# Optimization experiments

Hardware: AMD Instinct MI355X
Metric: run time of the kernel (lower is better)

Reference implementation:

```python
import jax, jax.numpy as jnp
import numpy as np

B = 4096          # batch_size * world_size
D = 256           # embedding dim
TEMP = 0.5        # temperature
EPS = 1e-8        # torch CosineSimilarity eps


def setup_inputs() -> dict:
    key = jax.random.key(0)
    k1, k2 = jax.random.split(key)
    z_i = jax.random.normal(k1, (B, D), dtype=jnp.float32)
    z_j = jax.random.normal(k2, (B, D), dtype=jnp.float32)
    return {"z_i": z_i, "z_j": z_j}


def reference(z_i, z_j):
    N = 2 * B
    z = jnp.concatenate([z_i, z_j], axis=0)                      # [N, D]
    # Cosine similarity: normalize rows (clamped norm like torch eps), then matmul.
    norms = jnp.maximum(jnp.linalg.norm(z, axis=1, keepdims=True), EPS)
    zn = z / norms
    sim = jnp.matmul(zn, zn.T) / TEMP                            # [N, N]
    # Positive pairs: offsets +B and -B from the diagonal.
    pos = jnp.concatenate([jnp.diagonal(sim, B), jnp.diagonal(sim, -B)])  # [N]
    # Cross-entropy with label 0 over [pos, negatives]:
    # logsumexp over {pos} U {negatives} == logsumexp over row excluding the diagonal
    # (the (i, i±B) entries removed by the mask are exactly re-added as the positive).
    neg_inf = jnp.array(-jnp.inf, dtype=sim.dtype)
    sim_nodiag = jnp.where(jnp.eye(N, dtype=bool), neg_inf, sim)
    lse = jax.nn.logsumexp(sim_nodiag, axis=1)                   # [N]
    loss = jnp.sum(lse - pos) / N                                # reduction='sum' then /N
    return loss
```

## Files before the change

### kernel.cpp

```cpp
#include <hip/hip_runtime.h>

#define NROWS 8192
#define DIM   256
#define BHALF 4096
#define NCHUNK 8
#define SCALE 1.69864358f
#define LN2F  0.69314718f

typedef unsigned char u8;
typedef __attribute__((ext_vector_type(4))) float f32x4;
typedef __attribute__((ext_vector_type(4))) int   i32x4;
typedef __attribute__((ext_vector_type(8))) int   i32x8;

__device__ inline void gload_lds16(const void* g, void* l) {
  __builtin_amdgcn_global_load_lds(
      (const __attribute__((address_space(1))) void*)g,
      (__attribute__((address_space(3))) void*)l, 16, 0, 0);
}

__global__ __launch_bounds__(256) void nrm_kernel(const float* __restrict__ zi,
                                                  const float* __restrict__ zj,
                                                  u8* __restrict__ zn8,
                                                  float* __restrict__ out) {
  if (blockIdx.x == 0 && threadIdx.x == 0) out[0] = 0.f;
  const int w = threadIdx.x >> 6, l = threadIdx.x & 63;
  const int row = blockIdx.x * 4 + w;
  const float* src = (row < BHALF) ? zi + (size_t)row * DIM
                                   : zj + (size_t)(row - BHALF) * DIM;
  float4 v = *(const float4*)(src + l * 4);
  float ss = v.x * v.x + v.y * v.y + v.z * v.z + v.w * v.w;
#pragma unroll
  for (int m = 1; m < 64; m <<= 1) ss += __shfl_xor(ss, m);
  float inv = SCALE / fmaxf(sqrtf(ss), 1e-8f);
  int p = __builtin_amdgcn_cvt_pk_fp8_f32(v.x * inv, v.y * inv, 0, false);
  p = __builtin_amdgcn_cvt_pk_fp8_f32(v.z * inv, v.w * inv, p, true);
  *(int*)(zn8 + (size_t)row * DIM + (size_t)l * 4) = p;
}

__global__ __launch_bounds__(256, 2) void sim_kernel(const u8* __restrict__ zn8,
                                                     float* __restrict__ partials,
                                                     float* __restrict__ pos) {
  __shared__ __align__(16) u8 Bsm[2][128 * DIM];
  __shared__ float plane[2][128];

  const int t = threadIdx.x;
  const int w = t >> 6, l = t & 63;
  const int wa = w >> 1, wb = w & 1;
  const int rl = l & 15, kg = l >> 4;

  const int rp = (int)blockIdx.x >> 3;
  const int ch = (int)blockIdx.x & 7;
  const int colbase = ch * 1024;

  int soff[8], doff[8];
#pragma unroll
  for (int i = 0; i < 8; ++i) {
    int c = i * 256 + t;
    int r = c >> 4, cd = c & 15;
    int cs = (cd & 8) | ((cd ^ r) & 7);
    soff[i] = r * DIM + cs * 16;
    doff[i] = (i * 256 + w * 64) * 16;
  }
  auto STAGE = [&](int base_row, u8* dst) {
#pragma unroll
    for (int i = 0; i < 8; ++i)
      gload_lds16(zn8 + (size_t)base_row * DIM + soff[i], dst + doff[i]);
  };
  auto RD2 = [&](const u8* buf, int row, i32x8* dst) {
    const int salt = row & 7;
    const u8* base = buf + row * DIM;
#pragma unroll
    for (int k = 0; k < 2; ++k) {
      i32x4 lo = *(const i32x4*)(base + ((k * 8 + ((kg * 2) ^ salt)) << 4));
      i32x4 hi = *(const i32x4*)(base + ((k * 8 + ((kg * 2 + 1) ^ salt)) << 4));
      dst[k] = __builtin_shufflevector(lo, hi, 0, 1, 2, 3, 4, 5, 6, 7);
    }
  };

  STAGE(rp * 128, &Bsm[0][0]);
  STAGE(colbase, &Bsm[1][0]);
  asm volatile("s_waitcnt vmcnt(8)" ::: "memory");
  __builtin_amdgcn_sched_barrier(0);
  __builtin_amdgcn_s_barrier();
  __builtin_amdgcn_sched_barrier(0);

  i32x8 pb[4][2];
#pragma unroll
  for (int pj = 0; pj < 4; ++pj)
    RD2(&Bsm[0][0], wb * 64 + pj * 16 + rl, pb[pj]);
  asm volatile("s_waitcnt lgkmcnt(0)" ::: "memory");
  __builtin_amdgcn_sched_barrier(0);

  const int dtile = ((rp >> 3) == ch) ? (rp & 7) : -1;
  const int pg = (rp < 32) ? (rp + 32) : (rp - 32);
  const int ptile = ((pg >> 3) == ch) ? (pg & 7) : -1;

  float rsum[4] = {0.f, 0.f, 0.f, 0.f};
  float pv[4]   = {0.f, 0.f, 0.f, 0.f};
  const bool dlane = (wa == wb) && (kg == (rl >> 2));
  const f32x4 z4 = {0.f, 0.f, 0.f, 0.f};

#pragma unroll 2
  for (int ti = 0; ti < 8; ++ti) {
    asm volatile("s_waitcnt vmcnt(0)" ::: "memory");
    __builtin_amdgcn_sched_barrier(0);
    __builtin_amdgcn_s_barrier();
    __builtin_amdgcn_sched_barrier(0);

    const u8* Bb = &Bsm[(ti + 1) & 1][0];
    if (ti < 7) STAGE(colbase + (ti + 1) * 128, &Bsm[ti & 1][0]);

    const bool tdiag = (ti == dtile), tpos = (ti == ptile);

    auto EPI = [&](int cip, const f32x4* a) {
#pragma unroll
      for (int pj = 0; pj < 4; ++pj)
#pragma unroll
        for (int jj = 0; jj < 4; ++jj)
          rsum[pj] += __builtin_amdgcn_exp2f(a[pj][jj]);
      if (tdiag && dlane)
        rsum[cip] -= __builtin_amdgcn_exp2f(a[cip][rl & 3]);
      if (tpos && dlane) pv[cip] = a[cip][rl & 3];
    };

    f32x4 acc[2][4];
    i32x8 af[2][2];
    RD2(Bb, wa * 64 + rl, af[0]);
#pragma unroll
    for (int ci = 0; ci < 4; ++ci) {
      if (ci < 3) RD2(Bb, wa * 64 + (ci + 1) * 16 + rl, af[(ci + 1) & 1]);
      if (ci < 3) asm volatile("s_waitcnt lgkmcnt(4)" ::: "memory");
      else        asm volatile("s_waitcnt lgkmcnt(0)" ::: "memory");
      __builtin_amdgcn_sched_barrier(0);

      __builtin_amdgcn_s_setprio(1);
#pragma unroll
      for (int pj = 0; pj < 4; ++pj)
        acc[ci & 1][pj] = __builtin_amdgcn_mfma_scale_f32_16x16x128_f8f6f4(
            af[ci & 1][0], pb[pj][0], z4,
            0, 0, 0, 0x7f7f7f7f, 0, 0x7f7f7f7f);
#pragma unroll
      for (int pj = 0; pj < 4; ++pj)
        acc[ci & 1][pj] = __builtin_amdgcn_mfma_scale_f32_16x16x128_f8f6f4(
            af[ci & 1][1], pb[pj][1], acc[ci & 1][pj],
            0, 0, 0, 0x7f7f7f7f, 0, 0x7f7f7f7f);
      __builtin_amdgcn_s_setprio(0);
      __builtin_amdgcn_sched_barrier(0);

      if (ci > 0) EPI(ci - 1, acc[(ci - 1) & 1]);
    }
    EPI(3, acc[1]);
  }

#pragma unroll
  for (int pj = 0; pj < 4; ++pj) {
    rsum[pj] += __shfl_xor(rsum[pj], 16);
    rsum[pj] += __shfl_xor(rsum[pj], 32);
  }
  if (kg == 0) {
#pragma unroll
    for (int pj = 0; pj < 4; ++pj)
      plane[wa][wb * 64 + pj * 16 + rl] = rsum[pj];
  }
  __syncthreads();
  if (t < 128)
    partials[(size_t)ch * NROWS + rp * 128 + t] = plane[0][t] + plane[1][t];
  if (ptile >= 0 && dlane) {
#pragma unroll
    for (int ci = 0; ci < 4; ++ci)
      pos[rp * 128 + wb * 64 + ci * 16 + rl] = pv[ci] * LN2F;
  }
}

__global__ __launch_bounds__(256) void fin_kernel(const float* __restrict__ partials,
                                                  const float* __restrict__ pos,
                                                  float* __restrict__ out) {
  const int r = blockIdx.x * 256 + threadIdx.x;
  float s = 0.f;
#pragma unroll
  for (int ch = 0; ch < NCHUNK; ++ch) s += partials[(size_t)ch * NROWS + r];
  float v = logf(s) - pos[r];
#pragma unroll
  for (int m = 1; m < 64; m <<= 1) v += __shfl_xor(v, m);
  __shared__ float wsum[4];
  const int w = threadIdx.x >> 6, l = threadIdx.x & 63;
  if (l == 0) wsum[w] = v;
  __syncthreads();
  if (threadIdx.x == 0)
    atomicAdd(out, (wsum[0] + wsum[1] + wsum[2] + wsum[3]) * (1.f / NROWS));
}

extern "C" void kernel_launch(void* const* d_in, const int* in_sizes, int n_in,
                              void* d_out, int out_size, void* d_ws, size_t ws_size,
                              hipStream_t stream) {
  const float* zi = (const float*)d_in[0];
  const float* zj = (const float*)d_in[1];

  u8*    zn8      = (u8*)d_ws;
  float* partials = (float*)((char*)d_ws + (size_t)NROWS * DIM);
  float* pos      = (float*)((char*)partials + (size_t)NCHUNK * NROWS * 4);
  float* out      = (float*)d_out;

  nrm_kernel<<<NROWS / 4, 256, 0, stream>>>(zi, zj, zn8, out);
  sim_kernel<<<64 * NCHUNK, 256, 0, stream>>>(zn8, partials, pos);
  fin_kernel<<<NROWS / 256, 256, 0, stream>>>(partials, pos, out);
}
```

Baseline: 32.07 us.

## Fuse final reduction into sim kernel via atomic counters and precompute positives

```diff
diff --git a/kernel.cpp b/kernel.cpp
--- a/kernel.cpp
+++ b/kernel.cpp
@@ -18,30 +18,79 @@
       (__attribute__((address_space(3))) void*)l, 16, 0, 0);
 }
 
+__device__ inline float fp8_to_f32(int b) {
+  const int e = (b >> 3) & 15, m = b & 7;
+  float mag = e ? __builtin_bit_cast(float, ((e + 120) << 23) | (m << 20))
+                : (float)m * 0x1p-9f;
+  return (b & 128) ? -mag : mag;
+}
+
 __global__ __launch_bounds__(256) void nrm_kernel(const float* __restrict__ zi,
                                                   const float* __restrict__ zj,
                                                   u8* __restrict__ zn8,
+                                                  float* __restrict__ rowsum,
+                                                  float* __restrict__ pos,
+                                                  float* __restrict__ diag,
+                                                  int* __restrict__ cnt,
                                                   float* __restrict__ out) {
-  if (blockIdx.x == 0 && threadIdx.x == 0) out[0] = 0.f;
-  const int w = threadIdx.x >> 6, l = threadIdx.x & 63;
-  const int row = blockIdx.x * 4 + w;
-  const float* src = (row < BHALF) ? zi + (size_t)row * DIM
-                                   : zj + (size_t)(row - BHALF) * DIM;
-  float4 v = *(const float4*)(src + l * 4);
-  float ss = v.x * v.x + v.y * v.y + v.z * v.z + v.w * v.w;
-#pragma unroll
-  for (int m = 1; m < 64; m <<= 1) ss += __shfl_xor(ss, m);
-  float inv = SCALE / fmaxf(sqrtf(ss), 1e-8f);
-  int p = __builtin_amdgcn_cvt_pk_fp8_f32(v.x * inv, v.y * inv, 0, false);
-  p = __builtin_amdgcn_cvt_pk_fp8_f32(v.z * inv, v.w * inv, p, true);
-  *(int*)(zn8 + (size_t)row * DIM + (size_t)l * 4) = p;
+  const int t = threadIdx.x, b = blockIdx.x;
+  const int gid = b * 256 + t;
+  if (gid < NROWS) rowsum[gid] = 0.f;
+  if (gid < 64) cnt[gid] = 0;
+  if (gid == 0) out[0] = 0.f;
+
+  const int w = t >> 6, l = t & 63;
+#pragma unroll
+  for (int q = 0; q < 2; ++q) {
+    const int p = b * 8 + w * 2 + q;
+    float4 vi = *(const float4*)(zi + (size_t)p * DIM + l * 4);
+    float4 vj = *(const float4*)(zj + (size_t)p * DIM + l * 4);
+    float ssi = vi.x * vi.x + vi.y * vi.y + vi.z * vi.z + vi.w * vi.w;
+    float ssj = vj.x * vj.x + vj.y * vj.y + vj.z * vj.z + vj.w * vj.w;
+#pragma unroll
+    for (int m = 1; m < 64; m <<= 1) {
+      ssi += __shfl_xor(ssi, m);
+      ssj += __shfl_xor(ssj, m);
+    }
+    const float invi = SCALE / fmaxf(sqrtf(ssi), 1e-8f);
+    const float invj = SCALE / fmaxf(sqrtf(ssj), 1e-8f);
+    int pi = __builtin_amdgcn_cvt_pk_fp8_f32(vi.x * invi, vi.y * invi, 0, false);
+    pi = __builtin_amdgcn_cvt_pk_fp8_f32(vi.z * invi, vi.w * invi, pi, true);
+    int pj = __builtin_amdgcn_cvt_pk_fp8_f32(vj.x * invj, vj.y * invj, 0, false);
+    pj = __builtin_amdgcn_cvt_pk_fp8_f32(vj.z * invj, vj.w * invj, pj, true);
+    *(int*)(zn8 + (size_t)p * DIM + l * 4) = pi;
+    *(int*)(zn8 + (size_t)(p + BHALF) * DIM + l * 4) = pj;
+
+    float dot = 0.f, di = 0.f, dj = 0.f;
+#pragma unroll
+    for (int k2 = 0; k2 < 4; ++k2) {
+      const float qi = fp8_to_f32((pi >> (8 * k2)) & 255);
+      const float qj = fp8_to_f32((pj >> (8 * k2)) & 255);
+      dot += qi * qj; di += qi * qi; dj += qj * qj;
+    }
+#pragma unroll
+    for (int m = 1; m < 64; m <<= 1) {
+      dot += __shfl_xor(dot, m);
+      di  += __shfl_xor(di, m);
+      dj  += __shfl_xor(dj, m);
+    }
+    if      (l == 0) pos[p] = dot * LN2F;
+    else if (l == 1) pos[p + BHALF] = dot * LN2F;
+    else if (l == 2) diag[p] = di;
+    else if (l == 3) diag[p + BHALF] = dj;
+  }
 }
 
 __global__ __launch_bounds__(256, 2) void sim_kernel(const u8* __restrict__ zn8,
-                                                     float* __restrict__ partials,
-                                                     float* __restrict__ pos) {
+                                                     float* __restrict__ rowsum,
+                                                     const float* __restrict__ pos,
+                                                     const float* __restrict__ diag,
+                                                     int* __restrict__ cnt,
+                                                     float* __restrict__ out) {
   __shared__ __align__(16) u8 Bsm[2][128 * DIM];
   __shared__ float plane[2][128];
+  __shared__ float wsum[2];
+  __shared__ int sfin;
 
   const int t = threadIdx.x;
   const int w = t >> 6, l = t & 63;
@@ -91,14 +140,16 @@
   asm volatile("s_waitcnt lgkmcnt(0)" ::: "memory");
   __builtin_amdgcn_sched_barrier(0);
 
-  const int dtile = ((rp >> 3) == ch) ? (rp & 7) : -1;
-  const int pg = (rp < 32) ? (rp + 32) : (rp - 32);
-  const int ptile = ((pg >> 3) == ch) ? (pg & 7) : -1;
-
   float rsum[4] = {0.f, 0.f, 0.f, 0.f};
-  float pv[4]   = {0.f, 0.f, 0.f, 0.f};
-  const bool dlane = (wa == wb) && (kg == (rl >> 2));
   const f32x4 z4 = {0.f, 0.f, 0.f, 0.f};
+
+  auto EPI = [&](const f32x4* a) {
+#pragma unroll
+    for (int pj = 0; pj < 4; ++pj)
+#pragma unroll
+      for (int jj = 0; jj < 4; ++jj)
+        rsum[pj] += __builtin_amdgcn_exp2f(a[pj][jj]);
+  };
 
 #pragma unroll 2
   for (int ti = 0; ti < 8; ++ti) {
@@ -110,19 +161,6 @@
     const u8* Bb = &Bsm[(ti + 1) & 1][0];
     if (ti < 7) STAGE(colbase + (ti + 1) * 128, &Bsm[ti & 1][0]);
 
-    const bool tdiag = (ti == dtile), tpos = (ti == ptile);
-
-    auto EPI = [&](int cip, const f32x4* a) {
-#pragma unroll
-      for (int pj = 0; pj < 4; ++pj)
-#pragma unroll
-        for (int jj = 0; jj < 4; ++jj)
-          rsum[pj] += __builtin_amdgcn_exp2f(a[pj][jj]);
-      if (tdiag && dlane)
-        rsum[cip] -= __builtin_amdgcn_exp2f(a[cip][rl & 3]);
-      if (tpos && dlane) pv[cip] = a[cip][rl & 3];
-    };
-
     f32x4 acc[2][4];
     i32x8 af[2][2];
     RD2(Bb, wa * 64 + rl, af[0]);
@@ -147,9 +185,9 @@
       __builtin_amdgcn_s_setprio(0);
       __builtin_amdgcn_sched_barrier(0);
 
-      if (ci > 0) EPI(ci - 1, acc[(ci - 1) & 1]);
-    }
-    EPI(3, acc[1]);
+      if (ci > 0) EPI(acc[(ci - 1) & 1]);
+    }
+    EPI(acc[1]);
   }
 
 #pragma unroll
@@ -163,31 +201,26 @@
       plane[wa][wb * 64 + pj * 16 + rl] = rsum[pj];
   }
   __syncthreads();
+
   if (t < 128)
-    partials[(size_t)ch * NROWS + rp * 128 + t] = plane[0][t] + plane[1][t];
-  if (ptile >= 0 && dlane) {
-#pragma unroll
-    for (int ci = 0; ci < 4; ++ci)
-      pos[rp * 128 + wb * 64 + ci * 16 + rl] = pv[ci] * LN2F;
-  }
-}
-
-__global__ __launch_bounds__(256) void fin_kernel(const float* __restrict__ partials,
-                                                  const float* __restrict__ pos,
-                                                  float* __restrict__ out) {
-  const int r = blockIdx.x * 256 + threadIdx.x;
-  float s = 0.f;
-#pragma unroll
-  for (int ch = 0; ch < NCHUNK; ++ch) s += partials[(size_t)ch * NROWS + r];
-  float v = logf(s) - pos[r];
-#pragma unroll
-  for (int m = 1; m < 64; m <<= 1) v += __shfl_xor(v, m);
-  __shared__ float wsum[4];
-  const int w = threadIdx.x >> 6, l = threadIdx.x & 63;
-  if (l == 0) wsum[w] = v;
+    atomicAdd(&rowsum[rp * 128 + t], plane[0][t] + plane[1][t]);
+  asm volatile("s_waitcnt vmcnt(0)" ::: "memory");
   __syncthreads();
-  if (threadIdx.x == 0)
-    atomicAdd(out, (wsum[0] + wsum[1] + wsum[2] + wsum[3]) * (1.f / NROWS));
+  if (t == 0) sfin = (atomicAdd(&cnt[rp], 1) == NCHUNK - 1);
+  __syncthreads();
+  if (sfin) {
+    float v = 0.f;
+    if (t < 128) {
+      const int r = rp * 128 + t;
+      float s = atomicAdd(&rowsum[r], 0.f);
+      v = logf(s - __builtin_amdgcn_exp2f(diag[r])) - pos[r];
+    }
+#pragma unroll
+    for (int m = 1; m < 64; m <<= 1) v += __shfl_xor(v, m);
+    if (l == 0 && t < 128) wsum[w] = v;
+    __syncthreads();
+    if (t == 0) atomicAdd(out, (wsum[0] + wsum[1]) * (1.f / NROWS));
+  }
 }
 
 extern "C" void kernel_launch(void* const* d_in, const int* in_sizes, int n_in,
@@ -196,12 +229,13 @@
   const float* zi = (const float*)d_in[0];
   const float* zj = (const float*)d_in[1];
 
-  u8*    zn8      = (u8*)d_ws;
-  float* partials = (float*)((char*)d_ws + (size_t)NROWS * DIM);
-  float* pos      = (float*)((char*)partials + (size_t)NCHUNK * NROWS * 4);
-  float* out      = (float*)d_out;
-
-  nrm_kernel<<<NROWS / 4, 256, 0, stream>>>(zi, zj, zn8, out);
-  sim_kernel<<<64 * NCHUNK, 256, 0, stream>>>(zn8, partials, pos);
-  fin_kernel<<<NROWS / 256, 256, 0, stream>>>(partials, pos, out);
-}
+  u8*    zn8    = (u8*)d_ws;
+  float* rowsum = (float*)((char*)d_ws + (size_t)NROWS * DIM);
+  float* pos    = (float*)((char*)rowsum + (size_t)NROWS * 4);
+  float* diag   = (float*)((char*)pos + (size_t)NROWS * 4);
+  int*   cnt    = (int*)((char*)diag + (size_t)NROWS * 4);
+  float* out    = (float*)d_out;
+
+  nrm_kernel<<<512, 256, 0, stream>>>(zi, zj, zn8, rowsum, pos, diag, cnt, out);
+  sim_kernel<<<64 * NCHUNK, 256, 0, stream>>>(zn8, rowsum, pos, diag, cnt, out);
+}
```

Result: no change. 31.81 us (-0.8%).
